# Kernel tuning notes

Measured on AMD Instinct MI355X. Metric: run time of the kernel, lower is better.

The kernel has to match this reference:

```python
import jax, jax.numpy as jnp
import numpy as np

# ViT-B on the Lorentz hyperboloid (curvature C): points x = [x_time, x_space],
# x_time = sqrt(||x_space||^2 + C). All linear/conv/norm ops act on the space
# part and recompute time; residuals/attention-midpoints renormalize the full
# Lorentz vector back onto the hyperboloid.
B, IMG, P, CIN, D, H, L = 32, 224, 16, 3, 768, 12, 12
HD = D // H          # per-head space dim (64)
DFF = 2048           # swiglu hidden: int(2/3 * 4*768) aligned to 64
C = 1.0
EPS = 1e-6


def _time(xs):
    return jnp.sqrt(jnp.clip(jnp.sum(xs * xs, -1, keepdims=True) + C, EPS, None))


def _to_lorentz(xs):
    return jnp.concatenate([_time(xs), xs], -1)


def _project(z):
    # renormalize full Lorentz vector so <z,z>_L = -C
    zz = jnp.sum(z[..., 1:] ** 2, -1, keepdims=True) - z[..., :1] ** 2
    return z * (jnp.sqrt(C) / jnp.sqrt(jnp.clip(-zz, EPS, None)))


def _lorentz_ln(x, g, b):
    xs = x[..., 1:]
    mu = xs.mean(-1, keepdims=True)
    var = ((xs - mu) ** 2).mean(-1, keepdims=True)
    xs = (xs - mu) / jnp.sqrt(var + 1e-6) * g + b
    return _to_lorentz(xs)


def _lresnet(x, y, w):
    # Lorentzian weighted residual: midpoint of x and w*y, projected to manifold
    return _project(x + w * y)


def _rope_tables():
    # 2D axial rope over the 14x14 patch grid, identity rotation for 1 cls token
    n = IMG // P
    d4 = HD // 4
    inv = 1.0 / (100.0 ** (np.arange(d4) / d4))
    ang = np.arange(n)[:, None] * inv[None, :]            # [n, d4]
    ay = np.repeat(ang[:, None, :], n, axis=1)            # row angles
    ax = np.repeat(ang[None, :, :], n, axis=0)            # col angles
    a = np.concatenate([ay, ax], -1).reshape(n * n, HD // 2)
    cos = np.concatenate([np.ones((1, HD // 2)), np.cos(a)], 0)
    sin = np.concatenate([np.zeros((1, HD // 2)), np.sin(a)], 0)
    return jnp.asarray(cos, jnp.float32), jnp.asarray(sin, jnp.float32)


def _apply_rope(x, cos, sin):
    # x: [B,N,H,HD]; rotate consecutive pairs (complex multiply)
    xr = x.reshape(*x.shape[:-1], -1, 2)
    x0, x1 = xr[..., 0], xr[..., 1]
    c = cos[None, :, None, :]
    s = sin[None, :, None, :]
    out = jnp.stack([x0 * c - x1 * s, x0 * s + x1 * c], -1)
    return out.reshape(x.shape)


def _attention(x, Wq, Wk, Wv, Wo, cos, sin, scale):
    b, n, _ = x.shape
    xs = x[..., 1:]
    q = (xs @ Wq).reshape(b, n, H, HD)
    k = (xs @ Wk).reshape(b, n, H, HD)
    v = (xs @ Wv).reshape(b, n, H, HD)
    q = _apply_rope(q, cos, sin)
    k = _apply_rope(k, cos, sin)
    qt = _time(q)[..., 0]   # [B,N,H]
    kt = _time(k)[..., 0]
    # Lorentz inner product <q,k>_L = -q_t k_t + q_s . k_s
    inner = jnp.einsum('bnhd,bmhd->bhnm', q, k) - jnp.einsum('bnh,bmh->bhnm', qt, kt)
    attn = jax.nn.softmax((2.0 * C + 2.0 * inner) / scale, axis=-1)
    vf = jnp.concatenate([_time(v), v], -1)               # [B,M,H,HD+1]
    mid = jnp.einsum('bhnm,bmhe->bnhe', attn, vf)         # Lorentzian midpoint
    mid = _project(mid)
    out_s = mid[..., 1:].reshape(b, n, H * HD) @ Wo       # concat heads + proj
    return _to_lorentz(out_s)


def setup_inputs() -> dict:
    key = jax.random.key(0)
    ks = jax.random.split(key, 12)
    std = 0.02
    nrm = lambda k, shape: jax.random.normal(k, shape, jnp.float32) * std
    return {
        'x': jax.random.normal(ks[0], (B, CIN, IMG, IMG), jnp.float32),
        'cls_s': nrm(ks[1], (D - 1,)),
        'Wp': nrm(ks[2], (P, P, CIN + 1, D - 1)),         # HWIO conv kernel
        'ln1_g': jnp.ones((L, D - 1), jnp.float32),
        'ln1_b': jnp.zeros((L, D - 1), jnp.float32),
        'Wq': nrm(ks[3], (L, D - 1, H * HD)),
        'Wk': nrm(ks[4], (L, D - 1, H * HD)),
        'Wv': nrm(ks[5], (L, D - 1, H * HD)),
        'Wo': nrm(ks[6], (L, H * HD, D - 1)),
        'ln2_g': jnp.ones((L, D - 1), jnp.float32),
        'ln2_b': jnp.zeros((L, D - 1), jnp.float32),
        'W1': nrm(ks[7], (L, D - 1, DFF)),
        'W2': nrm(ks[8], (L, D - 1, DFF)),
        'W3': nrm(ks[9], (L, DFF, D - 1)),
        'wy1': jnp.ones((L,), jnp.float32),
        'wy2': jnp.ones((L,), jnp.float32),
        'lnf_g': jnp.ones((D - 1,), jnp.float32),
        'lnf_b': jnp.zeros((D - 1,), jnp.float32),
    }


def reference(x, cls_s, Wp, ln1_g, ln1_b, Wq, Wk, Wv, Wo, ln2_g, ln2_b,
              W1, W2, W3, wy1, wy2, lnf_g, lnf_b):
    b = x.shape[0]
    xs = jnp.transpose(x, (0, 2, 3, 1))                   # BHWC
    xl = _to_lorentz(xs)                                  # pixel-wise time channel
    feat = jax.lax.conv_general_dilated(
        xl, Wp, (P, P), 'VALID',
        dimension_numbers=('NHWC', 'HWIO', 'NHWC'))       # [B,14,14,D-1]
    tok = _to_lorentz(feat).reshape(b, -1, D)             # [B,196,D]
    cls = jnp.broadcast_to(_to_lorentz(cls_s)[None, None, :], (b, 1, D))
    tok = jnp.concatenate([cls, tok], 1)                  # [B,197,D]
    cos, sin = _rope_tables()
    scale = jnp.sqrt(jnp.asarray(H * HD, jnp.float32))
    for l in range(L):
        xn = _lorentz_ln(tok, ln1_g[l], ln1_b[l])
        a = _attention(xn, Wq[l], Wk[l], Wv[l], Wo[l], cos, sin, scale)
        tok = _lresnet(tok, a, wy1[l])
        xn = _lorentz_ln(tok, ln2_g[l], ln2_b[l])
        hs = xn[..., 1:]
        m = _to_lorentz((jax.nn.silu(hs @ W1[l]) * (hs @ W2[l])) @ W3[l])
        tok = _lresnet(tok, m, wy2[l])
    return _lorentz_ln(tok, lnf_g, lnf_b)
```

## Files before the change

### kernel.cpp

```cpp
#include <hip/hip_runtime.h>
#include <hip/hip_bf16.h>

typedef __attribute__((ext_vector_type(8))) short short8;
typedef __attribute__((ext_vector_type(4))) float f32x4;
typedef _Float16 f16x8 __attribute__((ext_vector_type(8)));

#define NLAYER 12
#define NTOK   6304
#define MPAD   6400
#define CONVM  6272

#define QELE     ((size_t)384*208*64)
#define VELE     ((size_t)384*80*232)

static constexpr size_t AL(size_t x){ return (x + 511) & ~(size_t)511; }
static constexpr size_t B_COS    = 0;
static constexpr size_t B_SIN    = AL(B_COS    + (size_t)197*32*4);
static constexpr size_t B_WPT    = AL(B_SIN    + (size_t)197*32*4);
static constexpr size_t B_APATCH = AL(B_WPT    + (size_t)768*1024*2);
static constexpr size_t B_WQKVT  = AL(B_APATCH + (size_t)CONVM*1024*2);
static constexpr size_t B_WOT    = AL(B_WQKVT  + (size_t)2304*768*2);
static constexpr size_t B_W12T   = AL(B_WOT    + (size_t)768*768*2);
static constexpr size_t B_W3T    = AL(B_W12T   + (size_t)4096*768*2);
static constexpr size_t B_TOK    = AL(B_W3T    + (size_t)768*2048*2);
static constexpr size_t B_ACTA   = AL(B_TOK    + (size_t)NTOK*768*4);
static constexpr size_t B_ACTB   = AL(B_ACTA   + (size_t)MPAD*768*2);
static constexpr size_t B_GOUT   = AL(B_ACTB   + (size_t)MPAD*2048*2);
static constexpr size_t B_QB     = AL(B_GOUT   + (size_t)MPAD*2304*4);
static constexpr size_t B_KB     = AL(B_QB     + QELE*2);
static constexpr size_t B_VT     = AL(B_KB     + QELE*2);
static constexpr size_t B_QTB    = AL(B_VT     + VELE*2);
static constexpr size_t B_KTB    = AL(B_QTB    + (size_t)384*208*4);
static constexpr size_t B_END    = AL(B_KTB    + (size_t)384*208*4);

typedef __attribute__((address_space(1))) unsigned int gu32;
typedef __attribute__((address_space(3))) unsigned int lu32;
__device__ __forceinline__ void gld16(const void* g, void* l) {
  __builtin_amdgcn_global_load_lds((const gu32*)g, (lu32*)l, 16, 0, 0);
}

__device__ __forceinline__ float bsum(float v, float* red) {
  #pragma unroll
  for (int m = 32; m; m >>= 1) v += __shfl_xor(v, m, 64);
  __syncthreads();
  if ((threadIdx.x & 63) == 0) red[threadIdx.x >> 6] = v;
  __syncthreads();
  return red[0] + red[1] + red[2] + red[3];
}

__device__ __forceinline__ ushort h_us(float v) {
  _Float16 h = (_Float16)v;
  return *(ushort*)&h;
}

__global__ void k_rope_tab(float* __restrict__ cosb, float* __restrict__ sinb) {
  int idx = blockIdx.x * 256 + threadIdx.x;
  if (idx >= 197 * 32) return;
  int p = idx >> 5, j = idx & 31;
  float cv, sv;
  if (p == 0) { cv = 1.f; sv = 0.f; }
  else {
    int pp = p - 1;
    int iy = pp / 14, ix = pp - iy * 14;
    int pos = (j < 16) ? iy : ix;
    int f   = (j < 16) ? j  : j - 16;
    float inv = powf(100.f, -(float)f / 16.f);
    float a = (float)pos * inv;
    cv = cosf(a); sv = sinf(a);
  }
  cosb[idx] = cv; sinb[idx] = sv;
}

__device__ __forceinline__ void tpose_tile(const float* __restrict__ src, ushort* __restrict__ dst,
                                           int K, int N, int ldd, int imode, int tk, int tn) {
  __shared__ float ts[32][33];
  int t = threadIdx.x;
  int rr = t >> 3, c4 = (t & 7) * 4;
  int k0 = tk * 32, n0 = tn * 32;
  #pragma unroll
  for (int e = 0; e < 4; ++e) {
    int k = k0 + rr, n = n0 + c4 + e;
    ts[rr][c4 + e] = (k < K && n < N) ? src[(size_t)k * N + n] : 0.f;
  }
  __syncthreads();
  int c = n0 + rr;
  int drow = (imode == 0) ? c : (16 * (c >> 3) + (c & 7) + (imode == 2 ? 8 : 0));
  ushort4 o;
  #pragma unroll
  for (int e = 0; e < 4; ++e) {
    _Float16 hv = (_Float16)ts[c4 + e][rr];
    ((ushort*)&o)[e] = *(ushort*)&hv;
  }
  *(ushort4*)&dst[(size_t)drow * ldd + k0 + c4] = o;
}

__global__ __launch_bounds__(256) void k_tpose(const float* __restrict__ src, ushort* __restrict__ dst,
                                               int K, int N, int ktiles, int ldd) {
  int tk = blockIdx.x % ktiles, tn = blockIdx.x / ktiles;
  tpose_tile(src, dst, K, N, ldd, 0, tk, tn);
}

__global__ __launch_bounds__(256) void k_wprep(const float* __restrict__ Wq, const float* __restrict__ Wk,
                                               const float* __restrict__ Wv, const float* __restrict__ Wo,
                                               const float* __restrict__ W1, const float* __restrict__ W2,
                                               const float* __restrict__ W3,
                                               ushort* __restrict__ wqkvt, ushort* __restrict__ wot,
                                               ushort* __restrict__ w12t, ushort* __restrict__ w3t) {
  int tile = blockIdx.x;
  const float* src; ushort* dst;
  int K, N, ktiles, ldd, imode = 0, tl;
  if (tile < 2304) {
    int jb = tile / 576; tl = tile % 576;
    ktiles = 24; ldd = 768;
    if (jb == 0)      { src = Wq; dst = wqkvt;                 K = 767; N = 768; }
    else if (jb == 1) { src = Wk; dst = wqkvt + 768 * 768;     K = 767; N = 768; }
    else if (jb == 2) { src = Wv; dst = wqkvt + 2 * 768 * 768; K = 767; N = 768; }
    else              { src = Wo; dst = wot;                   K = 768; N = 767; }
  } else if (tile < 5376) {
    int jb = (tile - 2304) / 1536; tl = (tile - 2304) % 1536;
    ktiles = 24; ldd = 768; K = 767; N = 2048; dst = w12t;
    src = jb ? W2 : W1; imode = jb ? 2 : 1;
  } else {
    tl = tile - 5376; ktiles = 64; ldd = 2048; K = 2048; N = 767; src = W3; dst = w3t;
  }
  int tk = tl % ktiles, tn = tl / ktiles;
  tpose_tile(src, dst, K, N, ldd, imode, tk, tn);
}

__global__ __launch_bounds__(256) void k_im2col(const float* __restrict__ x, ushort* __restrict__ ap) {
  int r = blockIdx.x;
  int b = r / 196, pi = r - b * 196;
  int py = pi / 14, px = pi - py * 14;
  int t = threadIdx.x;
  int ph = t >> 4, pw = t & 15;
  int iy = py * 16 + ph, ix = px * 16 + pw;
  size_t base = ((size_t)b * 3 * 224 + iy) * 224 + ix;
  float x0 = x[base];
  float x1 = x[base + 224 * 224];
  float x2 = x[base + 2 * 224 * 224];
  float tv = sqrtf(fmaxf(x0 * x0 + x1 * x1 + x2 * x2 + 1.f, 1e-6f));
  size_t o = (size_t)r * 1024 + t * 4;
  ap[o] = h_us(tv); ap[o + 1] = h_us(x0); ap[o + 2] = h_us(x1); ap[o + 3] = h_us(x2);
}

template<int SILU>
__global__ __launch_bounds__(256) void k_gemmh(const ushort* __restrict__ A, const ushort* __restrict__ Bt,
                                               float* __restrict__ C, ushort* __restrict__ H,
                                               int N, int K) {
  __shared__ ushort sA[128 * 64];
  __shared__ ushort sB[128 * 64];
  int m0 = blockIdx.x * 128, n0 = blockIdx.y * 128;
  int t = threadIdx.x;
  int w = t >> 6, l = t & 63;
  int wm = (w >> 1) * 64, wn = (w & 1) * 64;
  int lr = l & 15, hi = l >> 4;
  f32x4 acc[4][4] = {};
  for (int k0 = 0; k0 < K; k0 += 64) {
    #pragma unroll
    for (int i = 0; i < 4; ++i) {
      int fl = i * 256 + t;
      int r = fl >> 3, c = fl & 7;
      int cs = c ^ (r & 7);
      gld16(&A[(size_t)(m0 + r) * K + k0 + cs * 8], &sA[fl * 8]);
      gld16(&Bt[(size_t)(n0 + r) * K + k0 + cs * 8], &sB[fl * 8]);
    }
    __syncthreads();
    f16x8 af[4][2], bfr[4][2];
    #pragma unroll
    for (int q = 0; q < 4; ++q) {
      int ra = wm + q * 16 + lr, rb = wn + q * 16 + lr;
      #pragma unroll
      for (int h = 0; h < 2; ++h) {
        af[q][h]  = *(const f16x8*)&sA[ra * 64 + ((h * 4 + hi) ^ (ra & 7)) * 8];
        bfr[q][h] = *(const f16x8*)&sB[rb * 64 + ((h * 4 + hi) ^ (rb & 7)) * 8];
      }
    }
    #pragma unroll
    for (int mi = 0; mi < 4; ++mi)
      #pragma unroll
      for (int ni = 0; ni < 4; ++ni) {
        acc[mi][ni] = __builtin_amdgcn_mfma_f32_16x16x32_f16(af[mi][0], bfr[ni][0], acc[mi][ni], 0, 0, 0);
        acc[mi][ni] = __builtin_amdgcn_mfma_f32_16x16x32_f16(af[mi][1], bfr[ni][1], acc[mi][ni], 0, 0, 0);
      }
    __syncthreads();
  }
  int rr = hi * 4, cc = lr;
  if (SILU) {
    #pragma unroll
    for (int mi = 0; mi < 4; ++mi)
      #pragma unroll
      for (int ni = 0; ni < 4; ++ni) {
        int g = (n0 + wn + ni * 16) >> 4;
        #pragma unroll
        for (int j = 0; j < 4; ++j) {
          float v = acc[mi][ni][j];
          float p = __shfl_xor(v, 8);
          float u1 = (cc < 8) ? v : p;
          float u2 = (cc < 8) ? p : v;
          float hv = u1 / (1.f + __expf(-u1)) * u2;
          if (cc < 8)
            H[(size_t)(m0 + wm + mi * 16 + rr + j) * 2048 + g * 8 + cc] = h_us(hv);
        }
      }
  } else {
    #pragma unroll
    for (int mi = 0; mi < 4; ++mi)
      #pragma unroll
      for (int ni = 0; ni < 4; ++ni)
        #pragma unroll
        for (int j = 0; j < 4; ++j)
          C[(size_t)(m0 + wm + mi * 16 + rr + j) * N + (n0 + wn + ni * 16 + cc)] = acc[mi][ni][j];
  }
}

__global__ __launch_bounds__(256) void k_build_tok(const float* __restrict__ feat, const float* __restrict__ cls,
                                                   float* __restrict__ tok) {
  __shared__ float red[8];
  int r = blockIdx.x;
  int b = r / 197, i = r - b * 197;
  int t = threadIdx.x;
  const float* src = (i == 0) ? cls : (feat + (size_t)(b * 196 + i - 1) * 768);
  float v0 = src[t], v1 = src[256 + t], v2 = (t < 255) ? src[512 + t] : 0.f;
  float qs = bsum(v0 * v0 + v1 * v1 + v2 * v2, red);
  float* tp = tok + (size_t)r * 768;
  if (t == 0) tp[0] = sqrtf(fmaxf(qs + 1.f, 1e-6f));
  tp[1 + t] = v0; tp[257 + t] = v1; if (t < 255) tp[513 + t] = v2;
}

__global__ __launch_bounds__(256) void k_ln(const float* __restrict__ tok, const float* __restrict__ g,
                                            const float* __restrict__ bb, ushort* __restrict__ out) {
  __shared__ float red[8];
  int r = blockIdx.x, t = threadIdx.x;
  const float* xp = tok + (size_t)r * 768;
  float v0 = xp[1 + t], v1 = xp[257 + t], v2 = (t < 255) ? xp[513 + t] : 0.f;
  float s = bsum(v0 + v1 + v2, red);
  float q = bsum(v0 * v0 + v1 * v1 + v2 * v2, red);
  float mu = s * (1.f / 767.f);
  float rstd = rsqrtf(fmaxf(q * (1.f / 767.f) - mu * mu, 0.f) + 1e-6f);
  size_t o = (size_t)r * 768;
  out[o + t]       = h_us((v0 - mu) * rstd * g[t]       + bb[t]);
  out[o + 256 + t] = h_us((v1 - mu) * rstd * g[256 + t] + bb[256 + t]);
  if (t < 255)
    out[o + 512 + t] = h_us((v2 - mu) * rstd * g[512 + t] + bb[512 + t]);
  if (t == 255) out[o + 767] = 0;
}

__global__ __launch_bounds__(384) void k_qkvpost(const float* __restrict__ qkv, const float* __restrict__ cosb,
                                                 const float* __restrict__ sinb,
                                                 ushort* __restrict__ qbuf, ushort* __restrict__ kbuf,
                                                 ushort* __restrict__ vtb,
                                                 float* __restrict__ qtb, float* __restrict__ ktb) {
  int r = blockIdx.x;
  int b = r / 197, n = r - b * 197;
  int t = threadIdx.x;
  int h = t >> 5, j = t & 31;
  const float* row = qkv + (size_t)r * 2304;
  float q0 = row[h * 64 + 2 * j],        q1 = row[h * 64 + 2 * j + 1];
  float k0 = row[768 + h * 64 + 2 * j],  k1 = row[768 + h * 64 + 2 * j + 1];
  float v0 = row[1536 + h * 64 + 2 * j], v1 = row[1536 + h * 64 + 2 * j + 1];
  float c = cosb[n * 32 + j], sn = sinb[n * 32 + j];
  float qa = q0 * c - q1 * sn, qc = q0 * sn + q1 * c;
  float ka = k0 * c - k1 * sn, kc = k0 * sn + k1 * c;
  float sq = q0 * q0 + q1 * q1, sk = k0 * k0 + k1 * k1, sv = v0 * v0 + v1 * v1;
  #pragma unroll
  for (int m = 16; m; m >>= 1) {
    sq += __shfl_xor(sq, m, 64);
    sk += __shfl_xor(sk, m, 64);
    sv += __shfl_xor(sv, m, 64);
  }
  int bh = b * 12 + h;
  size_t qo = ((size_t)bh * 208 + n) * 64 + 2 * j;
  qbuf[qo] = h_us(qa); qbuf[qo + 1] = h_us(qc);
  kbuf[qo] = h_us(ka); kbuf[qo + 1] = h_us(kc);
  size_t vo = (size_t)bh * 80 * 232;
  vtb[vo + (size_t)(1 + 2 * j) * 232 + n] = h_us(v0);
  vtb[vo + (size_t)(2 + 2 * j) * 232 + n] = h_us(v1);
  if (j == 0) {
    qtb[(size_t)bh * 208 + n] = sqrtf(fmaxf(sq + 1.f, 1e-6f));
    ktb[(size_t)bh * 208 + n] = sqrtf(fmaxf(sk + 1.f, 1e-6f));
    vtb[vo + n] = h_us(sqrtf(fmaxf(sv + 1.f, 1e-6f)));
  }
}

__global__ __launch_bounds__(128) void k_attn(const ushort* __restrict__ qbuf,
                                              const float* __restrict__ qtb,
                                              const ushort* __restrict__ kbuf,
                                              const float* __restrict__ ktb,
                                              const ushort* __restrict__ vtb,
                                              ushort* __restrict__ outa) {
  __shared__ ushort sK[208 * 72];
  __shared__ ushort sP[2][16 * 248];
  __shared__ float  sKt[208];
  int half = blockIdx.x, bh = blockIdx.y;
  int b = bh / 12, hd = bh - b * 12;
  int t = threadIdx.x, w = t >> 6, l = t & 63;
  const ushort* kg = kbuf + (size_t)bh * 208 * 64;
  for (int cks = t; cks < 1664; cks += 128) {
    int r = cks >> 3, c8 = (cks & 7) * 8;
    *(int4*)&sK[r * 72 + c8] = *(const int4*)&kg[r * 64 + c8];
  }
  for (int i = t; i < 208; i += 128) sKt[i] = ktb[(size_t)bh * 208 + i];
  __syncthreads();
  const ushort* qg = qbuf + (size_t)bh * 208 * 64;
  const ushort* vg = vtb + (size_t)bh * 80 * 232;
  const float invs = 0.03608439182435161f;
  int rt0 = half ? 7 : 0, rt1 = half ? 13 : 7;
  int lr = l & 15, hi4 = l >> 4;
  ushort* pw = &sP[w][0];
  for (int rt = rt0 + w; rt < rt1; rt += 2) {
    int qrow = (rt * 16 + lr) * 64 + hi4 * 8;
    f16x8 q0 = *(const f16x8*)&qg[qrow];
    f16x8 q1 = *(const f16x8*)&qg[qrow + 32];
    float qt4[4];
    #pragma unroll
    for (int j = 0; j < 4; ++j) qt4[j] = qtb[(size_t)bh * 208 + rt * 16 + hi4 * 4 + j];
    f32x4 acc[13];
    #pragma unroll
    for (int nt = 0; nt < 13; ++nt) {
      int kr = (nt * 16 + lr) * 72 + hi4 * 8;
      f16x8 k0 = *(const f16x8*)&sK[kr];
      f16x8 k1 = *(const f16x8*)&sK[kr + 32];
      acc[nt] = (f32x4){0.f, 0.f, 0.f, 0.f};
      acc[nt] = __builtin_amdgcn_mfma_f32_16x16x32_f16(q0, k0, acc[nt], 0, 0, 0);
      acc[nt] = __builtin_amdgcn_mfma_f32_16x16x32_f16(q1, k1, acc[nt], 0, 0, 0);
    }
    float mx[4] = {-1e30f, -1e30f, -1e30f, -1e30f};
    #pragma unroll
    for (int nt = 0; nt < 13; ++nt) {
      int cI = nt * 16 + lr;
      float ktc = sKt[cI];
      bool valid = (cI < 197);
      #pragma unroll
      for (int j = 0; j < 4; ++j) {
        float s = (2.f + 2.f * (acc[nt][j] - qt4[j] * ktc)) * invs;
        acc[nt][j] = s;
        if (valid) mx[j] = fmaxf(mx[j], s);
      }
    }
    #pragma unroll
    for (int j = 0; j < 4; ++j)
      #pragma unroll
      for (int m = 8; m; m >>= 1) mx[j] = fmaxf(mx[j], __shfl_xor(mx[j], m, 64));
    #pragma unroll
    for (int nt = 0; nt < 14; ++nt) {
      int cI = nt * 16 + lr;
      #pragma unroll
      for (int j = 0; j < 4; ++j) {
        float p = (nt < 13 && cI < 197) ? __expf(acc[nt][j] - mx[j]) : 0.f;
        pw[(hi4 * 4 + j) * 248 + cI] = h_us(p);
      }
    }
    f32x4 accO[5];
    #pragma unroll
    for (int et = 0; et < 5; ++et) accO[et] = (f32x4){0.f, 0.f, 0.f, 0.f};
    #pragma unroll
    for (int ks = 0; ks < 7; ++ks) {
      f16x8 pa = *(const f16x8*)&pw[lr * 248 + ks * 32 + hi4 * 8];
      #pragma unroll
      for (int et = 0; et < 5; ++et) {
        int er = et * 16 + lr;
        f16x8 bv = *(const f16x8*)&vg[(er > 64 ? 64 : er) * 232 + ks * 32 + hi4 * 8];
        accO[et] = __builtin_amdgcn_mfma_f32_16x16x32_f16(pa, bv, accO[et], 0, 0, 0);
      }
    }
    float ssq[4] = {0.f, 0.f, 0.f, 0.f};
    #pragma unroll
    for (int et = 0; et < 4; ++et)
      #pragma unroll
      for (int j = 0; j < 4; ++j) ssq[j] += accO[et][j] * accO[et][j];
    if (lr == 0) {
      #pragma unroll
      for (int j = 0; j < 4; ++j) ssq[j] += accO[4][j] * accO[4][j];
    }
    #pragma unroll
    for (int j = 0; j < 4; ++j)
      #pragma unroll
      for (int m = 8; m; m >>= 1) ssq[j] += __shfl_xor(ssq[j], m, 64);
    float rf4[4];
    #pragma unroll
    for (int j = 0; j < 4; ++j) {
      float o0 = __shfl(accO[0][j], (l & 48));
      rf4[j] = rsqrtf(fmaxf(2.f * o0 * o0 - ssq[j], 1e-6f));
    }
    #pragma unroll
    for (int et = 0; et < 5; ++et) {
      int e = et * 16 + lr;
      if (e == 0 || e >= 65) continue;
      #pragma unroll
      for (int j = 0; j < 4; ++j) {
        int n = rt * 16 + hi4 * 4 + j;
        if (n < 197)
          outa[((size_t)(b * 197 + n)) * 768 + hd * 64 + (e - 1)] = h_us(accO[et][j] * rf4[j]);
      }
    }
  }
}

template<int FIN>
__global__ __launch_bounds__(256) void k_resnet_ln(float* __restrict__ tok, const float* __restrict__ s,
                                                   const float* __restrict__ wyp, int l,
                                                   const float* __restrict__ g, const float* __restrict__ bb,
                                                   ushort* __restrict__ out16, float* __restrict__ out32) {
  __shared__ float red[8];
  __shared__ float bc[1];
  int r = blockIdx.x, t = threadIdx.x;
  float w = wyp[l];
  const float* sp = s + (size_t)r * 768;
  float* tp = tok + (size_t)r * 768;
  float s0 = sp[t], s1 = sp[256 + t], s2 = (t < 255) ? sp[512 + t] : 0.f;
  float qs = bsum(s0 * s0 + s1 * s1 + s2 * s2, red);
  float at = sqrtf(fmaxf(qs + 1.f, 1e-6f));
  float z0 = tp[1 + t] + w * s0;
  float z1 = tp[257 + t] + w * s1;
  float z2 = (t < 255) ? (tp[513 + t] + w * s2) : 0.f;
  float zs = bsum(z0 * z0 + z1 * z1 + z2 * z2, red);
  if (t == 0) bc[0] = tp[0] + w * at;
  __syncthreads();
  float zt = bc[0];
  float rf = rsqrtf(fmaxf(zt * zt - zs, 1e-6f));
  float n0 = z0 * rf, n1 = z1 * rf, n2 = z2 * rf;
  tp[1 + t] = n0; tp[257 + t] = n1; if (t < 255) tp[513 + t] = n2;
  if (t == 0) tp[0] = zt * rf;
  float sm = bsum(n0 + n1 + n2, red);
  float sq = bsum(n0 * n0 + n1 * n1 + n2 * n2, red);
  float mu = sm * (1.f / 767.f);
  float rstd = rsqrtf(fmaxf(sq * (1.f / 767.f) - mu * mu, 0.f) + 1e-6f);
  float y0 = (n0 - mu) * rstd * g[t] + bb[t];
  float y1 = (n1 - mu) * rstd * g[256 + t] + bb[256 + t];
  float y2 = (t < 255) ? ((n2 - mu) * rstd * g[512 + t] + bb[512 + t]) : 0.f;
  if (FIN) {
    float qq = bsum(y0 * y0 + y1 * y1 + y2 * y2, red);
    float* op = out32 + (size_t)r * 768;
    op[1 + t] = y0; op[257 + t] = y1; if (t < 255) op[513 + t] = y2;
    if (t == 0) op[0] = sqrtf(fmaxf(qq + 1.f, 1e-6f));
  } else {
    size_t o = (size_t)r * 768;
    out16[o + t] = h_us(y0);
    out16[o + 256 + t] = h_us(y1);
    if (t < 255) out16[o + 512 + t] = h_us(y2);
    if (t == 255) out16[o + 767] = 0;
  }
}

extern "C" void kernel_launch(void* const* d_in, const int* in_sizes, int n_in,
                              void* d_out, int out_size, void* d_ws, size_t ws_size,
                              hipStream_t stream) {
  const float* x     = (const float*)d_in[0];
  const float* cls_s = (const float*)d_in[1];
  const float* Wp    = (const float*)d_in[2];
  const float* ln1g  = (const float*)d_in[3];
  const float* ln1b  = (const float*)d_in[4];
  const float* Wq    = (const float*)d_in[5];
  const float* Wk    = (const float*)d_in[6];
  const float* Wv    = (const float*)d_in[7];
  const float* Wo    = (const float*)d_in[8];
  const float* ln2g  = (const float*)d_in[9];
  const float* ln2b  = (const float*)d_in[10];
  const float* W1    = (const float*)d_in[11];
  const float* W2    = (const float*)d_in[12];
  const float* W3    = (const float*)d_in[13];
  const float* wy1   = (const float*)d_in[14];
  const float* wy2   = (const float*)d_in[15];
  const float* lnfg  = (const float*)d_in[16];
  const float* lnfb  = (const float*)d_in[17];

  if (ws_size < B_END) return;

  char* ws = (char*)d_ws;
  float*  cosb   = (float*)(ws + B_COS);
  float*  sinb   = (float*)(ws + B_SIN);
  ushort* wpt    = (ushort*)(ws + B_WPT);
  ushort* apatch = (ushort*)(ws + B_APATCH);
  ushort* wqkvt  = (ushort*)(ws + B_WQKVT);
  ushort* wot    = (ushort*)(ws + B_WOT);
  ushort* w12t   = (ushort*)(ws + B_W12T);
  ushort* w3t    = (ushort*)(ws + B_W3T);
  float*  tok    = (float*)(ws + B_TOK);
  ushort* acta   = (ushort*)(ws + B_ACTA);
  ushort* actb   = (ushort*)(ws + B_ACTB);
  float*  gout   = (float*)(ws + B_GOUT);
  ushort* qbuf   = (ushort*)(ws + B_QB);
  ushort* kbuf   = (ushort*)(ws + B_KB);
  ushort* vtb    = (ushort*)(ws + B_VT);
  float*  qtb    = (float*)(ws + B_QTB);
  float*  ktb    = (float*)(ws + B_KTB);

  hipMemsetAsync(vtb, 0, VELE * 2, stream);

  k_rope_tab<<<25, 256, 0, stream>>>(cosb, sinb);
  k_tpose<<<32 * 24, 256, 0, stream>>>(Wp, wpt, 1024, 767, 32, 1024);
  k_im2col<<<CONVM, 256, 0, stream>>>(x, apatch);
  k_gemmh<0><<<dim3(49, 6), 256, 0, stream>>>(apatch, wpt, gout, nullptr, 768, 1024);
  k_build_tok<<<NTOK, 256, 0, stream>>>(gout, cls_s, tok);
  k_ln<<<NTOK, 256, 0, stream>>>(tok, ln1g, ln1b, acta);

  for (int l = 0; l < NLAYER; ++l) {
    k_wprep<<<6912, 256, 0, stream>>>(Wq + (size_t)l * 767 * 768, Wk + (size_t)l * 767 * 768,
                                      Wv + (size_t)l * 767 * 768, Wo + (size_t)l * 768 * 767,
                                      W1 + (size_t)l * 767 * 2048, W2 + (size_t)l * 767 * 2048,
                                      W3 + (size_t)l * 2048 * 767, wqkvt, wot, w12t, w3t);

    k_gemmh<0><<<dim3(50, 18), 256, 0, stream>>>(acta, wqkvt, gout, nullptr, 2304, 768);
    k_qkvpost<<<NTOK, 384, 0, stream>>>(gout, cosb, sinb, qbuf, kbuf, vtb, qtb, ktb);
    k_attn<<<dim3(2, 384), 128, 0, stream>>>(qbuf, qtb, kbuf, ktb, vtb, acta);
    k_gemmh<0><<<dim3(50, 6), 256, 0, stream>>>(acta, wot, gout, nullptr, 768, 768);
    k_resnet_ln<0><<<NTOK, 256, 0, stream>>>(tok, gout, wy1, l,
                                             ln2g + (size_t)l * 767, ln2b + (size_t)l * 767, acta, nullptr);

    k_gemmh<1><<<dim3(50, 32), 256, 0, stream>>>(acta, w12t, nullptr, actb, 4096, 768);
    k_gemmh<0><<<dim3(50, 6), 256, 0, stream>>>(actb, w3t, gout, nullptr, 768, 2048);
    if (l < NLAYER - 1)
      k_resnet_ln<0><<<NTOK, 256, 0, stream>>>(tok, gout, wy2, l,
                                               ln1g + (size_t)(l + 1) * 767, ln1b + (size_t)(l + 1) * 767,
                                               acta, nullptr);
    else
      k_resnet_ln<1><<<NTOK, 256, 0, stream>>>(tok, gout, wy2, l, lnfg, lnfb, nullptr, (float*)d_out);
  }
}
```

Measured before the change: 3.629 ms.

## Fuse QKV post-processing into GEMM epilogue and store projection outputs in fp16

The QKV GEMM gets a new epilogue mode that computes per-head Lorentz time norms, applies RoPE via lane shuffles, and writes q/k/v straight into the attention layouts. This removes the separate k_qkvpost kernel and the fp32 round-trip of the 2304-wide QKV output. The Wo and W3 GEMMs now write fp16 outputs that the residual/LN kernel reads, halving that traffic at the cost of lower precision in the residual branch. The fused epilogue does scattered global writes (transposed V, per-element stores) and reloads the cos/sin tables inside the epilogue.

```diff
diff --git a/kernel.cpp b/kernel.cpp
--- a/kernel.cpp
+++ b/kernel.cpp
@@ -51,6 +51,9 @@
 __device__ __forceinline__ ushort h_us(float v) {
   _Float16 h = (_Float16)v;
   return *(ushort*)&h;
+}
+__device__ __forceinline__ float us_f(ushort u) {
+  return (float)*(const _Float16*)&u;
 }
 
 __global__ void k_rope_tab(float* __restrict__ cosb, float* __restrict__ sinb) {
@@ -143,10 +146,14 @@
   ap[o] = h_us(tv); ap[o + 1] = h_us(x0); ap[o + 2] = h_us(x1); ap[o + 3] = h_us(x2);
 }
 
-template<int SILU>
+template<int MODE>
 __global__ __launch_bounds__(256) void k_gemmh(const ushort* __restrict__ A, const ushort* __restrict__ Bt,
                                                float* __restrict__ C, ushort* __restrict__ H,
-                                               int N, int K) {
+                                               int N, int K,
+                                               ushort* __restrict__ qbuf, ushort* __restrict__ kbuf,
+                                               ushort* __restrict__ vtb,
+                                               float* __restrict__ qtb, float* __restrict__ ktb,
+                                               const float* __restrict__ cosb, const float* __restrict__ sinb) {
   __shared__ ushort sA[128 * 64];
   __shared__ ushort sB[128 * 64];
   int m0 = blockIdx.x * 128, n0 = blockIdx.y * 128;
@@ -185,7 +192,7 @@
     __syncthreads();
   }
   int rr = hi * 4, cc = lr;
-  if (SILU) {
+  if (MODE == 1) {
     #pragma unroll
     for (int mi = 0; mi < 4; ++mi)
       #pragma unroll
@@ -202,6 +209,63 @@
             H[(size_t)(m0 + wm + mi * 16 + rr + j) * 2048 + g * 8 + cc] = h_us(hv);
         }
       }
+  } else if (MODE == 2) {
+    int secBase = n0 + wn;
+    int sec = secBase / 768;
+    int hh = (secBase - sec * 768) >> 6;
+    #pragma unroll
+    for (int mi = 0; mi < 4; ++mi) {
+      float nrm[4];
+      #pragma unroll
+      for (int j = 0; j < 4; ++j) {
+        float ss = 0.f;
+        #pragma unroll
+        for (int ni = 0; ni < 4; ++ni) ss += acc[mi][ni][j] * acc[mi][ni][j];
+        #pragma unroll
+        for (int m = 8; m; m >>= 1) ss += __shfl_xor(ss, m, 64);
+        nrm[j] = sqrtf(fmaxf(ss + 1.f, 1e-6f));
+      }
+      #pragma unroll
+      for (int j = 0; j < 4; ++j) {
+        int m = m0 + wm + mi * 16 + rr + j;
+        if (m < NTOK) {
+          int b = m / 197, nn = m - b * 197;
+          int bh = b * 12 + hh;
+          if (sec == 2) {
+            size_t vo = (size_t)bh * 80 * 232;
+            if (lr == 0) vtb[vo + nn] = h_us(nrm[j]);
+            #pragma unroll
+            for (int ni = 0; ni < 4; ++ni) {
+              int e = ni * 16 + lr;
+              vtb[vo + (size_t)(1 + e) * 232 + nn] = h_us(acc[mi][ni][j]);
+            }
+          } else {
+            float* tb = (sec == 0) ? qtb : ktb;
+            ushort* ob = (sec == 0) ? qbuf : kbuf;
+            if (lr == 0) tb[(size_t)bh * 208 + nn] = nrm[j];
+            size_t rowb = ((size_t)bh * 208 + nn) * 64;
+            #pragma unroll
+            for (int ni = 0; ni < 4; ++ni) {
+              int d = ni * 16 + lr;
+              float v = acc[mi][ni][j];
+              float p = __shfl_xor(v, 1);
+              int j2 = d >> 1;
+              float cz = cosb[nn * 32 + j2], sz = sinb[nn * 32 + j2];
+              float rv = ((lr & 1) == 0) ? (v * cz - p * sz) : (p * sz + v * cz);
+              ob[rowb + d] = h_us(rv);
+            }
+          }
+        }
+      }
+    }
+  } else if (MODE == 3) {
+    #pragma unroll
+    for (int mi = 0; mi < 4; ++mi)
+      #pragma unroll
+      for (int ni = 0; ni < 4; ++ni)
+        #pragma unroll
+        for (int j = 0; j < 4; ++j)
+          H[(size_t)(m0 + wm + mi * 16 + rr + j) * N + (n0 + wn + ni * 16 + cc)] = h_us(acc[mi][ni][j]);
   } else {
     #pragma unroll
     for (int mi = 0; mi < 4; ++mi)
@@ -245,43 +309,6 @@
   if (t == 255) out[o + 767] = 0;
 }
 
-__global__ __launch_bounds__(384) void k_qkvpost(const float* __restrict__ qkv, const float* __restrict__ cosb,
-                                                 const float* __restrict__ sinb,
-                                                 ushort* __restrict__ qbuf, ushort* __restrict__ kbuf,
-                                                 ushort* __restrict__ vtb,
-                                                 float* __restrict__ qtb, float* __restrict__ ktb) {
-  int r = blockIdx.x;
-  int b = r / 197, n = r - b * 197;
-  int t = threadIdx.x;
-  int h = t >> 5, j = t & 31;
-  const float* row = qkv + (size_t)r * 2304;
-  float q0 = row[h * 64 + 2 * j],        q1 = row[h * 64 + 2 * j + 1];
-  float k0 = row[768 + h * 64 + 2 * j],  k1 = row[768 + h * 64 + 2 * j + 1];
-  float v0 = row[1536 + h * 64 + 2 * j], v1 = row[1536 + h * 64 + 2 * j + 1];
-  float c = cosb[n * 32 + j], sn = sinb[n * 32 + j];
-  float qa = q0 * c - q1 * sn, qc = q0 * sn + q1 * c;
-  float ka = k0 * c - k1 * sn, kc = k0 * sn + k1 * c;
-  float sq = q0 * q0 + q1 * q1, sk = k0 * k0 + k1 * k1, sv = v0 * v0 + v1 * v1;
-  #pragma unroll
-  for (int m = 16; m; m >>= 1) {
-    sq += __shfl_xor(sq, m, 64);
-    sk += __shfl_xor(sk, m, 64);
-    sv += __shfl_xor(sv, m, 64);
-  }
-  int bh = b * 12 + h;
-  size_t qo = ((size_t)bh * 208 + n) * 64 + 2 * j;
-  qbuf[qo] = h_us(qa); qbuf[qo + 1] = h_us(qc);
-  kbuf[qo] = h_us(ka); kbuf[qo + 1] = h_us(kc);
-  size_t vo = (size_t)bh * 80 * 232;
-  vtb[vo + (size_t)(1 + 2 * j) * 232 + n] = h_us(v0);
-  vtb[vo + (size_t)(2 + 2 * j) * 232 + n] = h_us(v1);
-  if (j == 0) {
-    qtb[(size_t)bh * 208 + n] = sqrtf(fmaxf(sq + 1.f, 1e-6f));
-    ktb[(size_t)bh * 208 + n] = sqrtf(fmaxf(sk + 1.f, 1e-6f));
-    vtb[vo + n] = h_us(sqrtf(fmaxf(sv + 1.f, 1e-6f)));
-  }
-}
-
 __global__ __launch_bounds__(128) void k_attn(const ushort* __restrict__ qbuf,
                                               const float* __restrict__ qtb,
                                               const ushort* __restrict__ kbuf,
@@ -397,7 +424,7 @@
 }
 
 template<int FIN>
-__global__ __launch_bounds__(256) void k_resnet_ln(float* __restrict__ tok, const float* __restrict__ s,
+__global__ __launch_bounds__(256) void k_resnet_ln(float* __restrict__ tok, const ushort* __restrict__ s,
                                                    const float* __restrict__ wyp, int l,
                                                    const float* __restrict__ g, const float* __restrict__ bb,
                                                    ushort* __restrict__ out16, float* __restrict__ out32) {
@@ -405,9 +432,9 @@
   __shared__ float bc[1];
   int r = blockIdx.x, t = threadIdx.x;
   float w = wyp[l];
-  const float* sp = s + (size_t)r * 768;
+  const ushort* sp = s + (size_t)r * 768;
   float* tp = tok + (size_t)r * 768;
-  float s0 = sp[t], s1 = sp[256 + t], s2 = (t < 255) ? sp[512 + t] : 0.f;
+  float s0 = us_f(sp[t]), s1 = us_f(sp[256 + t]), s2 = (t < 255) ? us_f(sp[512 + t]) : 0.f;
   float qs = bsum(s0 * s0 + s1 * s1 + s2 * s2, red);
   float at = sqrtf(fmaxf(qs + 1.f, 1e-6f));
   float z0 = tp[1 + t] + w * s0;
@@ -479,6 +506,7 @@
   ushort* acta   = (ushort*)(ws + B_ACTA);
   ushort* actb   = (ushort*)(ws + B_ACTB);
   float*  gout   = (float*)(ws + B_GOUT);
+  ushort* gouth  = (ushort*)(ws + B_GOUT);
   ushort* qbuf   = (ushort*)(ws + B_QB);
   ushort* kbuf   = (ushort*)(ws + B_KB);
   ushort* vtb    = (ushort*)(ws + B_VT);
@@ -490,7 +518,8 @@
   k_rope_tab<<<25, 256, 0, stream>>>(cosb, sinb);
   k_tpose<<<32 * 24, 256, 0, stream>>>(Wp, wpt, 1024, 767, 32, 1024);
   k_im2col<<<CONVM, 256, 0, stream>>>(x, apatch);
-  k_gemmh<0><<<dim3(49, 6), 256, 0, stream>>>(apatch, wpt, gout, nullptr, 768, 1024);
+  k_gemmh<0><<<dim3(49, 6), 256, 0, stream>>>(apatch, wpt, gout, nullptr, 768, 1024,
+                                              nullptr, nullptr, nullptr, nullptr, nullptr, nullptr, nullptr);
   k_build_tok<<<NTOK, 256, 0, stream>>>(gout, cls_s, tok);
   k_ln<<<NTOK, 256, 0, stream>>>(tok, ln1g, ln1b, acta);
 
@@ -500,20 +529,23 @@
                                       W1 + (size_t)l * 767 * 2048, W2 + (size_t)l * 767 * 2048,
                                       W3 + (size_t)l * 2048 * 767, wqkvt, wot, w12t, w3t);
 
-    k_gemmh<0><<<dim3(50, 18), 256, 0, stream>>>(acta, wqkvt, gout, nullptr, 2304, 768);
-    k_qkvpost<<<NTOK, 384, 0, stream>>>(gout, cosb, sinb, qbuf, kbuf, vtb, qtb, ktb);
+    k_gemmh<2><<<dim3(50, 18), 256, 0, stream>>>(acta, wqkvt, nullptr, nullptr, 2304, 768,
+                                                 qbuf, kbuf, vtb, qtb, ktb, cosb, sinb);
     k_attn<<<dim3(2, 384), 128, 0, stream>>>(qbuf, qtb, kbuf, ktb, vtb, acta);
-    k_gemmh<0><<<dim3(50, 6), 256, 0, stream>>>(acta, wot, gout, nullptr, 768, 768);
-    k_resnet_ln<0><<<NTOK, 256, 0, stream>>>(tok, gout, wy1, l,
+    k_gemmh<3><<<dim3(50, 6), 256, 0, stream>>>(acta, wot, nullptr, gouth, 768, 768,
+                                                nullptr, nullptr, nullptr, nullptr, nullptr, nullptr, nullptr);
+    k_resnet_ln<0><<<NTOK, 256, 0, stream>>>(tok, gouth, wy1, l,
                                              ln2g + (size_t)l * 767, ln2b + (size_t)l * 767, acta, nullptr);
 
-    k_gemmh<1><<<dim3(50, 32), 256, 0, stream>>>(acta, w12t, nullptr, actb, 4096, 768);
-    k_gemmh<0><<<dim3(50, 6), 256, 0, stream>>>(actb, w3t, gout, nullptr, 768, 2048);
+    k_gemmh<1><<<dim3(50, 32), 256, 0, stream>>>(acta, w12t, nullptr, actb, 4096, 768,
+                                                 nullptr, nullptr, nullptr, nullptr, nullptr, nullptr, nullptr);
+    k_gemmh<3><<<dim3(50, 6), 256, 0, stream>>>(actb, w3t, nullptr, gouth, 768, 2048,
+                                                nullptr, nullptr, nullptr, nullptr, nullptr, nullptr, nullptr);
     if (l < NLAYER - 1)
-      k_resnet_ln<0><<<NTOK, 256, 0, stream>>>(tok, gout, wy2, l,
+      k_resnet_ln<0><<<NTOK, 256, 0, stream>>>(tok, gouth, wy2, l,
                                                ln1g + (size_t)(l + 1) * 767, ln1b + (size_t)(l + 1) * 767,
                                                acta, nullptr);
     else
-      k_resnet_ln<1><<<NTOK, 256, 0, stream>>>(tok, gout, wy2, l, lnfg, lnfb, nullptr, (float*)d_out);
-  }
-}
+      k_resnet_ln<1><<<NTOK, 256, 0, stream>>>(tok, gouth, wy2, l, lnfg, lnfb, nullptr, (float*)d_out);
+  }
+}
```

New measurement: 3.338 ms. -8.0%, faster.
